# Kernel optimization log

Hardware: AMD Instinct MI355X
Metric: run time of the kernel (lower is better)

## Reference

```python
import jax, jax.numpy as jnp
import numpy as np

DT = 0.042      # RON integration step
GAMMA = 2.7     # oscillator stiffness
EPS = 4.7       # oscillator damping
RHO_M = 1.0     # inter-module spectral-radius scaling
M, H, I, T = 16, 256, 128, 256


def _normalized_wm(rng):
    # matches __init__: uniform(-2,2) then divide each (H,H) block by its spectral radius, * rho_m
    wm = rng.uniform(-2.0, 2.0, size=(M, M, H, H)).astype(np.float32)
    flat = wm.reshape(M * M, H, H)
    srad = np.abs(np.linalg.eigvals(flat)).max(axis=1).astype(np.float32)  # (M*M,)
    wm = flat / srad[:, None, None] * RHO_M
    return jnp.asarray(wm.reshape(M, M, H, H))


def setup_inputs() -> dict:
    key = jax.random.key(0)
    ks = jax.random.split(key, 6)
    rng = np.random.default_rng(0)
    x = jax.random.normal(ks[0], (T, I), dtype=jnp.float32)
    wm = _normalized_wm(rng)
    conn = jax.random.randint(ks[1], (M, M), 0, 2).astype(jnp.float32)
    input_mask = jnp.ones((M,), dtype=jnp.float32)
    W_in = jax.random.normal(ks[2], (M, H, I), dtype=jnp.float32) / np.sqrt(I)
    W_rec = jax.random.normal(ks[3], (M, H, H), dtype=jnp.float32) / np.sqrt(H)
    bias = jax.random.normal(ks[4], (M, H), dtype=jnp.float32) * 0.1
    return {"x": x, "wm": wm, "connection_weights": conn, "input_mask": input_mask,
            "W_in": W_in, "W_rec": W_rec, "bias": bias}


def reference(x, wm, connection_weights, input_mask, W_in, W_rec, bias):
    m, h = wm.shape[0], wm.shape[2]
    scaling = 1.0 / jnp.clip(connection_weights.sum(axis=1), 1.0)  # (M,)

    def step(carry, x_t):
        states, outs = carry                      # (M,2,H), (M,H)
        hy, hz = states[:, 0], states[:, 1]
        # fused feedback matmul + connection masking + scaling:
        # fb[i,h1] = scaling[i] * sum_{o,h2} conn[i,o] * wm[i,o,h1,h2] * outs[o,h2]
        fb = jnp.einsum('io,iohg,og->ih', connection_weights, wm, outs) * scaling[:, None]
        u = input_mask[:, None] * x_t[None, :]    # (M,I) input broadcast per module
        pre = (jnp.einsum('mhi,mi->mh', W_in, u)
               + jnp.einsum('mhg,mg->mh', W_rec, hy)
               + bias + fb)
        hz_n = hz + DT * (jnp.tanh(pre) - GAMMA * hy - EPS * hz)
        hy_n = hy + DT * hz_n
        states_n = jnp.stack([hy_n, hz_n], axis=1)  # (M,2,H)
        return (states_n, hy_n), (states_n, fb)

    init = (jnp.zeros((m, 2, h), dtype=x.dtype), jnp.zeros((m, h), dtype=x.dtype))
    _, (state_seq, fb_seq) = jax.lax.scan(step, init, x)
    return state_seq, fb_seq  # (T,M,2,H), (T,M,H)
```

## Files before the change

### kernel.cpp

```cpp
#include <hip/hip_runtime.h>
#include <math.h>


#define DT_C    0.042f
#define GAMMA_C 2.7f
#define EPS_C   4.7f

constexpr int M = 16, H = 256, I = 128, T = 256;
constexpr int HP = H + 4;
constexpr int NROW = M * H;
constexpr int NBLK = 256;
constexpr int NTHR = 1024;
constexpr int NREPF = 16;

typedef float f32x4 __attribute__((ext_vector_type(4)));
typedef unsigned long long u64;
typedef unsigned int u32;

__device__ __align__(64) u64 g_hy[(size_t)(T + 1) * NROW];
__device__ __align__(64) u32 g_done[NREPF][NBLK];
__device__ u32 g_epoch;

__global__ __launch_bounds__(NTHR) void rnn_persistent(
    const float* __restrict__ x,
    const float* __restrict__ wm,
    const float* __restrict__ conn,
    const float* __restrict__ mask,
    const float* __restrict__ W_in,
    const float* __restrict__ W_rec,
    const float* __restrict__ bias,
    float* __restrict__ out)
{
  const int h    = blockIdx.x;
  const int tid  = threadIdx.x;
  const int m    = tid >> 6;
  const int lane = tid & 63;

  __shared__ float hy_lds[2][M * HP];
  __shared__ float outb_hz[T][M];
  __shared__ float outb_fb[T][M];
  __shared__ u64   s_pub[M];
  __shared__ float s_c[M * M];
  __shared__ float s_scal[M];
  __shared__ int   s_olist[M][M];
  __shared__ float s_oc[M][M];
  __shared__ int   s_ocnt[M];
  __shared__ u32   s_base;
  __shared__ u32   s_go;

  if (tid == 0) {
    s_base = __hip_atomic_load(&g_epoch, __ATOMIC_RELAXED, __HIP_MEMORY_SCOPE_AGENT);
    s_go = 0;
  }
  if (tid < M) s_pub[tid] = 0ull;
  if (tid < M * M) s_c[tid] = conn[tid];
  __syncthreads();

  const u32 base = s_base;
  if (tid < M) {
    const u64 pkt0 = ((u64)(base + 1u) << 32);
    __hip_atomic_store(&g_hy[(size_t)h * M + tid], pkt0,
                       __ATOMIC_RELAXED, __HIP_MEMORY_SCOPE_AGENT);
  }
  if (tid < NREPF)
    __hip_atomic_store(&g_done[tid][h], base + 1u,
                       __ATOMIC_RELAXED, __HIP_MEMORY_SCOPE_AGENT);

  if (tid < M) {
    float s = 0.f; int cnt = 0;
    for (int o = 0; o < M; ++o) {
      float c = s_c[tid * M + o];
      s += c;
      if (c != 0.f) { s_olist[tid][cnt] = o; s_oc[tid][cnt] = c; ++cnt; }
    }
    for (int k = cnt; k < M; ++k) { s_olist[tid][k] = 0; s_oc[tid][k] = 0.f; }
    s_ocnt[tid] = cnt;
    s_scal[tid] = 1.0f / fmaxf(s, 1.0f);
  }
  __syncthreads();

  const int   rowg  = m * H + h;
  const float maskm = mask[m];
  const float biasv = bias[rowg];
  const float scal  = s_scal[m];
  const int   ocnt  = s_ocnt[m];

  f32x4 wreg[M];
#pragma unroll
  for (int k = 0; k < M; ++k) {
    if (k < ocnt) {
      const int o = s_olist[m][k];
      const f32x4 wv = *reinterpret_cast<const f32x4*>(
          wm + ((size_t)(m * M + o) * H + h) * H + 4 * lane);
      wreg[k] = wv * s_oc[m][k];
    } else {
      wreg[k] = (f32x4)0.f;
    }
  }
  const f32x4  wrec = *reinterpret_cast<const f32x4*>(W_rec + (size_t)rowg * H + 4 * lane);
  const float2 win  = *reinterpret_cast<const float2*>(W_in + (size_t)rowg * I + 2 * lane);

  float hz = 0.f;
  float2 xd = *reinterpret_cast<const float2*>(x + 2 * lane);

  const int  mcol = (tid & 15) * HP;
  const int  hrow = tid >> 4;
  int buf = 0;

  for (int t = 0; t < T; ++t) {
    const u32 tgt = base + (u32)t + 1u;

    if (m == 0) {
      const u32* fp = &g_done[h & (NREPF - 1)][0] + lane;
      for (;;) {
        const u32 c0 = __hip_atomic_load(fp,       __ATOMIC_RELAXED, __HIP_MEMORY_SCOPE_AGENT);
        const u32 c1 = __hip_atomic_load(fp + 64,  __ATOMIC_RELAXED, __HIP_MEMORY_SCOPE_AGENT);
        const u32 c2 = __hip_atomic_load(fp + 128, __ATOMIC_RELAXED, __HIP_MEMORY_SCOPE_AGENT);
        const u32 c3 = __hip_atomic_load(fp + 192, __ATOMIC_RELAXED, __HIP_MEMORY_SCOPE_AGENT);
        const bool ok = (c0 >= tgt) & (c1 >= tgt) & (c2 >= tgt) & (c3 >= tgt);
        if (__all(ok)) break;
        __builtin_amdgcn_s_sleep(1);
      }
      if (lane == 0)
        __hip_atomic_store(&s_go, (u32)(t + 1), __ATOMIC_RELAXED,
                           __HIP_MEMORY_SCOPE_WORKGROUP);
    } else {
      while (__hip_atomic_load(&s_go, __ATOMIC_RELAXED,
                               __HIP_MEMORY_SCOPE_WORKGROUP) < (u32)(t + 1)) { }
    }
    asm volatile("" ::: "memory");

    {
      const u64* src = g_hy + (size_t)t * NROW + tid;
      u64 a0 = __hip_atomic_load(src,        __ATOMIC_RELAXED, __HIP_MEMORY_SCOPE_AGENT);
      u64 a1 = __hip_atomic_load(src + 1024, __ATOMIC_RELAXED, __HIP_MEMORY_SCOPE_AGENT);
      u64 a2 = __hip_atomic_load(src + 2048, __ATOMIC_RELAXED, __HIP_MEMORY_SCOPE_AGENT);
      u64 a3 = __hip_atomic_load(src + 3072, __ATOMIC_RELAXED, __HIP_MEMORY_SCOPE_AGENT);
      while (!((((u32)(a0 >> 32)) >= tgt) & (((u32)(a1 >> 32)) >= tgt) &
               (((u32)(a2 >> 32)) >= tgt) & (((u32)(a3 >> 32)) >= tgt))) {
        __builtin_amdgcn_s_sleep(1);
        a0 = __hip_atomic_load(src,        __ATOMIC_RELAXED, __HIP_MEMORY_SCOPE_AGENT);
        a1 = __hip_atomic_load(src + 1024, __ATOMIC_RELAXED, __HIP_MEMORY_SCOPE_AGENT);
        a2 = __hip_atomic_load(src + 2048, __ATOMIC_RELAXED, __HIP_MEMORY_SCOPE_AGENT);
        a3 = __hip_atomic_load(src + 3072, __ATOMIC_RELAXED, __HIP_MEMORY_SCOPE_AGENT);
      }
      float* dst = &hy_lds[buf][0];
      dst[mcol + hrow      ] = __uint_as_float((u32)a0);
      dst[mcol + hrow +  64] = __uint_as_float((u32)a1);
      dst[mcol + hrow + 128] = __uint_as_float((u32)a2);
      dst[mcol + hrow + 192] = __uint_as_float((u32)a3);
    }
    __syncthreads();

    float acc_o = win.x * (maskm * xd.x);
    acc_o = fmaf(win.y, maskm * xd.y, acc_o);
    {
      const f32x4 hp = *reinterpret_cast<const f32x4*>(&hy_lds[buf][m * HP + 4 * lane]);
      acc_o = fmaf(wrec.x, hp.x, acc_o);
      acc_o = fmaf(wrec.y, hp.y, acc_o);
      acc_o = fmaf(wrec.z, hp.z, acc_o);
      acc_o = fmaf(wrec.w, hp.w, acc_o);
    }
    float acc_fb = 0.f;
#pragma unroll
    for (int k = 0; k < M; ++k) {
      if (k < ocnt) {
        const int o = s_olist[m][k];
        const f32x4 hp = *reinterpret_cast<const f32x4*>(&hy_lds[buf][o * HP + 4 * lane]);
        float po = wreg[k].x * hp.x;
        po = fmaf(wreg[k].y, hp.y, po);
        po = fmaf(wreg[k].z, hp.z, po);
        po = fmaf(wreg[k].w, hp.w, po);
        acc_fb += po;
      }
    }

    for (int off = 32; off > 0; off >>= 1) {
      acc_fb += __shfl_xor(acc_fb, off);
      acc_o  += __shfl_xor(acc_o,  off);
    }

    if (lane == 0) {
      const float fb   = scal * acc_fb;
      const float hy_p = hy_lds[buf][m * HP + h];
      const float pre  = acc_o + biasv + fb;
      const float hz_n = hz + DT_C * (tanhf(pre) - GAMMA_C * hy_p - EPS_C * hz);
      const float hy_n = hy_p + DT_C * hz_n;
      hz = hz_n;
      const u64 pkt = ((u64)(tgt + 1u) << 32) | (u64)__float_as_uint(hy_n);
      __hip_atomic_store(&s_pub[m], pkt, __ATOMIC_RELAXED,
                         __HIP_MEMORY_SCOPE_WORKGROUP);
      outb_hz[t][m] = hz_n;
      outb_fb[t][m] = fb;
    }
    asm volatile("" ::: "memory");

    if (m == 0) {
      u64 p;
      for (;;) {
        p = __hip_atomic_load(&s_pub[lane & 15], __ATOMIC_RELAXED,
                              __HIP_MEMORY_SCOPE_WORKGROUP);
        if (__all(((u32)(p >> 32)) >= tgt + 1u)) break;
      }
      if (lane < M)
        __hip_atomic_store(&g_hy[(size_t)(t + 1) * NROW + (size_t)h * M + lane],
                           p, __ATOMIC_RELAXED, __HIP_MEMORY_SCOPE_AGENT);
      if (lane < NREPF)
        __hip_atomic_store(&g_done[lane][h], tgt + 1u,
                           __ATOMIC_RELAXED, __HIP_MEMORY_SCOPE_AGENT);
    }

    if (t + 1 < T)
      xd = *reinterpret_cast<const float2*>(x + (size_t)(t + 1) * I + 2 * lane);
    buf ^= 1;
  }

  __syncthreads();

  const size_t fb_base = (size_t)T * M * 2 * H;
  for (int i = tid; i < T * M; i += NTHR) {
    const int t  = i >> 4;
    const int mm = i & 15;
    const u64 q = __hip_atomic_load(
        &g_hy[(size_t)(t + 1) * NROW + (size_t)h * M + mm],
        __ATOMIC_RELAXED, __HIP_MEMORY_SCOPE_AGENT);
    const float hyv = __uint_as_float((u32)q);
    const size_t so = (size_t)t * (M * 2 * H) + (size_t)mm * (2 * H);
    out[so + h]     = hyv;
    out[so + H + h] = outb_hz[t][mm];
    out[fb_base + (size_t)t * (M * H) + (size_t)mm * H + h] = outb_fb[t][mm];
  }

  if (h == 0 && tid == 0)
    __hip_atomic_store(&g_epoch, base + (u32)(T + 2),
                       __ATOMIC_RELAXED, __HIP_MEMORY_SCOPE_AGENT);
}

extern "C" void kernel_launch(void* const* d_in, const int* in_sizes, int n_in,
                              void* d_out, int out_size, void* d_ws, size_t ws_size,
                              hipStream_t stream) {
  const float* x     = (const float*)d_in[0];
  const float* wm    = (const float*)d_in[1];
  const float* conn  = (const float*)d_in[2];
  const float* mask  = (const float*)d_in[3];
  const float* W_in  = (const float*)d_in[4];
  const float* W_rec = (const float*)d_in[5];
  const float* bias  = (const float*)d_in[6];

  rnn_persistent<<<NBLK, NTHR, 0, stream>>>(
      x, wm, conn, mask, W_in, W_rec, bias, (float*)d_out);
}
```

Baseline: 1.191 ms.

## Split per-step grid barrier into four quarter flags to overlap state loads

The single per-block go flag is replaced by four flags, one for each quarter of the 256 producer blocks. As soon as one quarter of the producers has published step t, every wave starts loading the matching 1024-element slice of the shared hidden state. The goal is to overlap global-memory latency with waiting for slower producers instead of waiting for the whole grid first. In exchange, the spin logic becomes more complex, waiting waves now sleep, and the flag polling adds more branches, which may increase per-step overhead.

```diff
diff --git a/kernel.cpp b/kernel.cpp
--- a/kernel.cpp
+++ b/kernel.cpp
@@ -46,12 +46,11 @@
   __shared__ float s_oc[M][M];
   __shared__ int   s_ocnt[M];
   __shared__ u32   s_base;
-  __shared__ u32   s_go;
-
-  if (tid == 0) {
+  __shared__ u32   s_gog[4];
+
+  if (tid == 0)
     s_base = __hip_atomic_load(&g_epoch, __ATOMIC_RELAXED, __HIP_MEMORY_SCOPE_AGENT);
-    s_go = 0;
-  }
+  if (tid < 4) s_gog[tid] = 0;
   if (tid < M) s_pub[tid] = 0ull;
   if (tid < M * M) s_c[tid] = conn[tid];
   __syncthreads();
@@ -109,33 +108,67 @@
 
   for (int t = 0; t < T; ++t) {
     const u32 tgt = base + (u32)t + 1u;
+    const u64* src = g_hy + (size_t)t * NROW + tid;
+    u64 a0 = 0, a1 = 0, a2 = 0, a3 = 0;
 
     if (m == 0) {
       const u32* fp = &g_done[h & (NREPF - 1)][0] + lane;
-      for (;;) {
+      u32 pend = 0xFu;
+      do {
         const u32 c0 = __hip_atomic_load(fp,       __ATOMIC_RELAXED, __HIP_MEMORY_SCOPE_AGENT);
         const u32 c1 = __hip_atomic_load(fp + 64,  __ATOMIC_RELAXED, __HIP_MEMORY_SCOPE_AGENT);
         const u32 c2 = __hip_atomic_load(fp + 128, __ATOMIC_RELAXED, __HIP_MEMORY_SCOPE_AGENT);
         const u32 c3 = __hip_atomic_load(fp + 192, __ATOMIC_RELAXED, __HIP_MEMORY_SCOPE_AGENT);
-        const bool ok = (c0 >= tgt) & (c1 >= tgt) & (c2 >= tgt) & (c3 >= tgt);
-        if (__all(ok)) break;
-        __builtin_amdgcn_s_sleep(1);
-      }
-      if (lane == 0)
-        __hip_atomic_store(&s_go, (u32)(t + 1), __ATOMIC_RELAXED,
-                           __HIP_MEMORY_SCOPE_WORKGROUP);
+        if ((pend & 1u) && __all(c0 >= tgt)) {
+          if (lane == 0)
+            __hip_atomic_store(&s_gog[0], (u32)(t + 1), __ATOMIC_RELAXED,
+                               __HIP_MEMORY_SCOPE_WORKGROUP);
+          a0 = __hip_atomic_load(src, __ATOMIC_RELAXED, __HIP_MEMORY_SCOPE_AGENT);
+          pend &= ~1u;
+        }
+        if ((pend & 2u) && __all(c1 >= tgt)) {
+          if (lane == 0)
+            __hip_atomic_store(&s_gog[1], (u32)(t + 1), __ATOMIC_RELAXED,
+                               __HIP_MEMORY_SCOPE_WORKGROUP);
+          a1 = __hip_atomic_load(src + 1024, __ATOMIC_RELAXED, __HIP_MEMORY_SCOPE_AGENT);
+          pend &= ~2u;
+        }
+        if ((pend & 4u) && __all(c2 >= tgt)) {
+          if (lane == 0)
+            __hip_atomic_store(&s_gog[2], (u32)(t + 1), __ATOMIC_RELAXED,
+                               __HIP_MEMORY_SCOPE_WORKGROUP);
+          a2 = __hip_atomic_load(src + 2048, __ATOMIC_RELAXED, __HIP_MEMORY_SCOPE_AGENT);
+          pend &= ~4u;
+        }
+        if ((pend & 8u) && __all(c3 >= tgt)) {
+          if (lane == 0)
+            __hip_atomic_store(&s_gog[3], (u32)(t + 1), __ATOMIC_RELAXED,
+                               __HIP_MEMORY_SCOPE_WORKGROUP);
+          a3 = __hip_atomic_load(src + 3072, __ATOMIC_RELAXED, __HIP_MEMORY_SCOPE_AGENT);
+          pend &= ~8u;
+        }
+      } while (pend);
     } else {
-      while (__hip_atomic_load(&s_go, __ATOMIC_RELAXED,
-                               __HIP_MEMORY_SCOPE_WORKGROUP) < (u32)(t + 1)) { }
+      while (__hip_atomic_load(&s_gog[0], __ATOMIC_RELAXED,
+                               __HIP_MEMORY_SCOPE_WORKGROUP) < (u32)(t + 1))
+        __builtin_amdgcn_s_sleep(1);
+      a0 = __hip_atomic_load(src, __ATOMIC_RELAXED, __HIP_MEMORY_SCOPE_AGENT);
+      while (__hip_atomic_load(&s_gog[1], __ATOMIC_RELAXED,
+                               __HIP_MEMORY_SCOPE_WORKGROUP) < (u32)(t + 1))
+        __builtin_amdgcn_s_sleep(1);
+      a1 = __hip_atomic_load(src + 1024, __ATOMIC_RELAXED, __HIP_MEMORY_SCOPE_AGENT);
+      while (__hip_atomic_load(&s_gog[2], __ATOMIC_RELAXED,
+                               __HIP_MEMORY_SCOPE_WORKGROUP) < (u32)(t + 1))
+        __builtin_amdgcn_s_sleep(1);
+      a2 = __hip_atomic_load(src + 2048, __ATOMIC_RELAXED, __HIP_MEMORY_SCOPE_AGENT);
+      while (__hip_atomic_load(&s_gog[3], __ATOMIC_RELAXED,
+                               __HIP_MEMORY_SCOPE_WORKGROUP) < (u32)(t + 1))
+        __builtin_amdgcn_s_sleep(1);
+      a3 = __hip_atomic_load(src + 3072, __ATOMIC_RELAXED, __HIP_MEMORY_SCOPE_AGENT);
     }
     asm volatile("" ::: "memory");
 
     {
-      const u64* src = g_hy + (size_t)t * NROW + tid;
-      u64 a0 = __hip_atomic_load(src,        __ATOMIC_RELAXED, __HIP_MEMORY_SCOPE_AGENT);
-      u64 a1 = __hip_atomic_load(src + 1024, __ATOMIC_RELAXED, __HIP_MEMORY_SCOPE_AGENT);
-      u64 a2 = __hip_atomic_load(src + 2048, __ATOMIC_RELAXED, __HIP_MEMORY_SCOPE_AGENT);
-      u64 a3 = __hip_atomic_load(src + 3072, __ATOMIC_RELAXED, __HIP_MEMORY_SCOPE_AGENT);
       while (!((((u32)(a0 >> 32)) >= tgt) & (((u32)(a1 >> 32)) >= tgt) &
                (((u32)(a2 >> 32)) >= tgt) & (((u32)(a3 >> 32)) >= tgt))) {
         __builtin_amdgcn_s_sleep(1);
```

Result: faster. 1.054 ms (-11.5%).

## Replace block-wide flag gate with per-wave partial readiness polling

Applied to the files above, without the earlier changes.

Drops the wave-0 global flag poll and LDS go-flag broadcast. Each wave now polls only the done flags of the 16 producer blocks whose data it will read, and issues each of its four hy loads as soon as that chunk's producers are ready. This is meant to remove the serialized two-level wait and let loads overlap with still-arriving producers. In exchange all 16 waves now poll global memory, which raises flag traffic. The original tag check on the packets remains as a safety net.

```diff
diff --git a/kernel.cpp b/kernel.cpp
--- a/kernel.cpp
+++ b/kernel.cpp
@@ -46,12 +46,9 @@
   __shared__ float s_oc[M][M];
   __shared__ int   s_ocnt[M];
   __shared__ u32   s_base;
-  __shared__ u32   s_go;
-
-  if (tid == 0) {
+
+  if (tid == 0)
     s_base = __hip_atomic_load(&g_epoch, __ATOMIC_RELAXED, __HIP_MEMORY_SCOPE_AGENT);
-    s_go = 0;
-  }
   if (tid < M) s_pub[tid] = 0ull;
   if (tid < M * M) s_c[tid] = conn[tid];
   __syncthreads();
@@ -105,37 +102,43 @@
 
   const int  mcol = (tid & 15) * HP;
   const int  hrow = tid >> 4;
+  const u32* fpw = &g_done[(h + m) & (NREPF - 1)]
+                          [4 * m + (lane & 3) + 64 * ((lane >> 2) & 3)];
   int buf = 0;
 
   for (int t = 0; t < T; ++t) {
     const u32 tgt = base + (u32)t + 1u;
-
-    if (m == 0) {
-      const u32* fp = &g_done[h & (NREPF - 1)][0] + lane;
-      for (;;) {
-        const u32 c0 = __hip_atomic_load(fp,       __ATOMIC_RELAXED, __HIP_MEMORY_SCOPE_AGENT);
-        const u32 c1 = __hip_atomic_load(fp + 64,  __ATOMIC_RELAXED, __HIP_MEMORY_SCOPE_AGENT);
-        const u32 c2 = __hip_atomic_load(fp + 128, __ATOMIC_RELAXED, __HIP_MEMORY_SCOPE_AGENT);
-        const u32 c3 = __hip_atomic_load(fp + 192, __ATOMIC_RELAXED, __HIP_MEMORY_SCOPE_AGENT);
-        const bool ok = (c0 >= tgt) & (c1 >= tgt) & (c2 >= tgt) & (c3 >= tgt);
-        if (__all(ok)) break;
-        __builtin_amdgcn_s_sleep(1);
-      }
-      if (lane == 0)
-        __hip_atomic_store(&s_go, (u32)(t + 1), __ATOMIC_RELAXED,
-                           __HIP_MEMORY_SCOPE_WORKGROUP);
-    } else {
-      while (__hip_atomic_load(&s_go, __ATOMIC_RELAXED,
-                               __HIP_MEMORY_SCOPE_WORKGROUP) < (u32)(t + 1)) { }
+    const u64* src = g_hy + (size_t)t * NROW + tid;
+    u64 a0 = 0, a1 = 0, a2 = 0, a3 = 0;
+
+    {
+      u32 pend = 0xFu;
+      do {
+        const u32 f = __hip_atomic_load(fpw, __ATOMIC_RELAXED,
+                                        __HIP_MEMORY_SCOPE_AGENT);
+        const u64 rdy = __ballot(f >= tgt);
+        if ((pend & 1u) && ((rdy & 0xFull) == 0xFull)) {
+          a0 = __hip_atomic_load(src, __ATOMIC_RELAXED, __HIP_MEMORY_SCOPE_AGENT);
+          pend &= ~1u;
+        }
+        if ((pend & 2u) && (((rdy >> 4) & 0xFull) == 0xFull)) {
+          a1 = __hip_atomic_load(src + 1024, __ATOMIC_RELAXED, __HIP_MEMORY_SCOPE_AGENT);
+          pend &= ~2u;
+        }
+        if ((pend & 4u) && (((rdy >> 8) & 0xFull) == 0xFull)) {
+          a2 = __hip_atomic_load(src + 2048, __ATOMIC_RELAXED, __HIP_MEMORY_SCOPE_AGENT);
+          pend &= ~4u;
+        }
+        if ((pend & 8u) && (((rdy >> 12) & 0xFull) == 0xFull)) {
+          a3 = __hip_atomic_load(src + 3072, __ATOMIC_RELAXED, __HIP_MEMORY_SCOPE_AGENT);
+          pend &= ~8u;
+        }
+        if (pend) __builtin_amdgcn_s_sleep(1);
+      } while (pend);
     }
     asm volatile("" ::: "memory");
 
     {
-      const u64* src = g_hy + (size_t)t * NROW + tid;
-      u64 a0 = __hip_atomic_load(src,        __ATOMIC_RELAXED, __HIP_MEMORY_SCOPE_AGENT);
-      u64 a1 = __hip_atomic_load(src + 1024, __ATOMIC_RELAXED, __HIP_MEMORY_SCOPE_AGENT);
-      u64 a2 = __hip_atomic_load(src + 2048, __ATOMIC_RELAXED, __HIP_MEMORY_SCOPE_AGENT);
-      u64 a3 = __hip_atomic_load(src + 3072, __ATOMIC_RELAXED, __HIP_MEMORY_SCOPE_AGENT);
       while (!((((u32)(a0 >> 32)) >= tgt) & (((u32)(a1 >> 32)) >= tgt) &
                (((u32)(a2 >> 32)) >= tgt) & (((u32)(a3 >> 32)) >= tgt))) {
         __builtin_amdgcn_s_sleep(1);
```

Measured after the change: 1.839 ms. 54.4% more time.
